# Optimization experiments

Hardware: AMD Instinct MI355X
Metric: run time of the kernel (lower is better)

## Reference

```python
import jax, jax.numpy as jnp
import numpy as np
from math import sqrt

B, N, DK = 4, 4096, 64


def setup_inputs() -> dict:
    key = jax.random.key(0)
    ks = jax.random.split(key, 5)
    x = jax.random.normal(ks[0], (B, N, DK), dtype=jnp.float32)
    Wv = jax.random.normal(ks[1], (DK, DK), dtype=jnp.float32) / sqrt(DK)
    bv = jax.random.normal(ks[2], (DK,), dtype=jnp.float32) * 0.02
    wq = jax.random.normal(ks[3], (DK,), dtype=jnp.float32) / sqrt(DK)
    wk = jax.random.normal(ks[4], (DK,), dtype=jnp.float32) / sqrt(DK)
    gamma = jnp.ones((DK,), dtype=jnp.float32)
    beta = jnp.zeros((DK,), dtype=jnp.float32)
    return {"x": x, "Wv": Wv, "bv": bv, "wq": wq, "wk": wk, "gamma": gamma, "beta": beta}


def _layer_norm(h, gamma, beta, eps=1e-5):
    mu = jnp.mean(h, axis=-1, keepdims=True)
    var = jnp.var(h, axis=-1, keepdims=True)
    return (h - mu) * jax.lax.rsqrt(var + eps) * gamma + beta


def reference(x, Wv, bv, wq, wk, gamma, beta):
    d_k = x.shape[-1]
    V = jnp.einsum('bnd,ed->bne', x, Wv) + bv          # (B, N, DK)
    Q = jnp.einsum('bnd,d->bn', x, wq)                 # scalar per token
    K = jnp.einsum('bnd,d->bn', x, wk)
    # RBF-kernel scores A[b,i,j] = exp(-(Q_i - K_j)^2)  -> (B, N, N)
    A = jnp.exp(-jnp.square(Q[:, :, None] - K[:, None, :]))
    P = jax.nn.softmax(A / sqrt(d_k), axis=-1)
    out = jnp.einsum('bij,bjd->bid', P, V) + x
    return _layer_norm(out, gamma, beta)
```

## Files before the change

kernel.cpp:

```cpp
#include <hip/hip_runtime.h>

#define NB   4
#define NSEQ 4096
#define DK   64
#define NTOK (NB * NSEQ)

#define QK_SCALE 1.2011224087864498f

typedef __attribute__((ext_vector_type(8))) short short8;
typedef __attribute__((ext_vector_type(4))) float f32x4;

__device__ __forceinline__ float fast_exp2(float x) {
#if __has_builtin(__builtin_amdgcn_exp2f)
    return __builtin_amdgcn_exp2f(x);
#else
    return exp2f(x);
#endif
}

__device__ __forceinline__ unsigned short bf16_rne(float f) {
    unsigned u = __float_as_uint(f);
    u += 0x7fffu + ((u >> 16) & 1u);
    return (unsigned short)(u >> 16);
}

__device__ __forceinline__ short8 u4_to_s8(uint4 u) {
    union { uint4 u; short8 s; } c; c.u = u; return c.s;
}

#define AS3U(p) ((__attribute__((address_space(3))) unsigned int*)(p))
#define AS1U(p) ((const __attribute__((address_space(1))) unsigned int*)(p))


__global__ __launch_bounds__(512) void qkv_kernel(
    const float* __restrict__ x, const float* __restrict__ Wv,
    const float* __restrict__ bv, const float* __restrict__ wq,
    const float* __restrict__ wk,
    float* __restrict__ Qs, float* __restrict__ Ks, unsigned short* __restrict__ Vt)
{
    __shared__ float x_lds[64 * 68];
    __shared__ float wvt[64 * 68];
    __shared__ float wqk[128];
    __shared__ float bvl[64];
    __shared__ unsigned short vt_lds[64 * 72];

    const int t = threadIdx.x;
    const int tok0 = blockIdx.x * 64;

    #pragma unroll
    for (int r = 0; r < 2; ++r) {
        int f = t + 512 * r;
        int row = f >> 4, c4 = f & 15;
        float4 v = ((const float4*)(x + (size_t)(tok0 + row) * DK))[c4];
        *(float4*)&x_lds[row * 68 + c4 * 4] = v;
    }
    #pragma unroll
    for (int r = 0; r < 2; ++r) {
        int f = t + 512 * r;
        int e = f >> 4, c4 = f & 15;
        float4 v = ((const float4*)(Wv + e * DK))[c4];
        wvt[(c4 * 4 + 0) * 68 + e] = v.x;
        wvt[(c4 * 4 + 1) * 68 + e] = v.y;
        wvt[(c4 * 4 + 2) * 68 + e] = v.z;
        wvt[(c4 * 4 + 3) * 68 + e] = v.w;
    }
    if (t < 64) { wqk[t * 2] = wq[t]; wqk[t * 2 + 1] = wk[t]; bvl[t] = bv[t]; }
    __syncthreads();

    const int tok = t >> 3, oc = t & 7;
    const int e0 = oc * 8;
    float acc[8];
    #pragma unroll
    for (int ee = 0; ee < 8; ++ee) acc[ee] = bvl[e0 + ee];

    for (int d = 0; d < DK; d += 4) {
        float4 x4 = *(const float4*)&x_lds[tok * 68 + d];
        const float xs[4] = {x4.x, x4.y, x4.z, x4.w};
        #pragma unroll
        for (int dd = 0; dd < 4; ++dd) {
            float xv = xs[dd];
            const float4* wrow = (const float4*)&wvt[(d + dd) * 68 + e0];
            float4 wa = wrow[0], wb = wrow[1];
            acc[0] += xv * wa.x; acc[1] += xv * wa.y;
            acc[2] += xv * wa.z; acc[3] += xv * wa.w;
            acc[4] += xv * wb.x; acc[5] += xv * wb.y;
            acc[6] += xv * wb.z; acc[7] += xv * wb.w;
        }
    }
    #pragma unroll
    for (int k = 0; k < 8; ++k)
        vt_lds[(e0 + k) * 72 + tok] = bf16_rne(acc[k]);

    if (t < 128) {
        const int tk = t & 63;
        const int sel = (t >= 64);
        float a = 0.f;
        for (int d = 0; d < DK; ++d)
            a += x_lds[tk * 68 + d] * wqk[d * 2 + sel];
        (sel ? Ks : Qs)[tok0 + tk] = a * QK_SCALE;
    }
    __syncthreads();

    const int bb = tok0 >> 12, n0 = tok0 & 4095;
    {
        const int c = t >> 6, d = t & 63;
        uint4 v = *(const uint4*)((const char*)vt_lds + d * 144 + c * 16);
        const int jc   = (n0 >> 5) + (c >> 2);
        const int lane = (c & 3) * 16 + (d & 15);
        const int ct   = d >> 4;
        unsigned short* dst = Vt + ((((size_t)bb * 128 + jc) * 4 + ct) * 64 + lane) * 8;
        *(uint4*)dst = v;
    }
}

extern __shared__ float smem[];

__global__ __launch_bounds__(1024, 4) void attn_kernel(
    const float* __restrict__ x,
    const float* __restrict__ Qsg, const float* __restrict__ Ksg,
    const unsigned short* __restrict__ Vt,
    const float* __restrict__ gamma, const float* __restrict__ beta,
    float* __restrict__ out, int nrep)
{
    float* k_lds = smem;
    unsigned short* vs = (unsigned short*)(smem + 4096);
    float* red   = smem + 4096;
    float* dred  = smem + 4096 + 8 * 64 * 68;

    const int t    = threadIdx.x;
    const int B    = blockIdx.x;
    const int b    = (B & 7) >> 1;
    const int i0   = (((B >> 3) << 1) | (B & 1)) << 6;
    const int w    = t >> 6;
    const int lane = t & 63;
    const int rit  = lane & 15;
    const int q    = lane >> 4;
    const int rgrp = w >> 3;
    const int js   = w & 7;

    ((float4*)k_lds)[t] = ((const float4*)(Ksg + (size_t)b * 4096))[t];

    const float Qs0 = Qsg[b * 4096 + i0 + rgrp * 32 + rit];
    const float Qs1 = Qsg[b * 4096 + i0 + rgrp * 32 + 16 + rit];

    const short onebf = (short)0x3F80;
    const short8 vones = {onebf, onebf, onebf, onebf, onebf, onebf, onebf, onebf};

    const unsigned short* Vtb0 = Vt + (size_t)b * 262144;

    for (int rep = 0; rep < nrep; ++rep) {

    f32x4 acc[2][4] = {};
    f32x4 accd[2] = {};

    #pragma unroll
    for (int i = 0; i < 4; ++i) {
        const int row = w + 16 * i;
        const unsigned short* g = Vtb0 + row * 512 + lane * 8;
        unsigned short* l = vs + row * 512;
#if __has_builtin(__builtin_amdgcn_global_load_lds)
        __builtin_amdgcn_global_load_lds(AS1U(g), AS3U(l), 16, 0, 0);
#else
        *(uint4*)(l + lane * 8) = *(const uint4*)g;
#endif
    }
    __syncthreads();

    for (int r = 0; r < 8; ++r) {
        const int bf = r & 1;
        if (r < 7) {
            #pragma unroll
            for (int i = 0; i < 4; ++i) {
                const int row = w + 16 * i;
                const unsigned short* g = Vtb0 + (r + 1) * 32768 + row * 512 + lane * 8;
                unsigned short* l = vs + (bf ^ 1) * 32768 + row * 512;
#if __has_builtin(__builtin_amdgcn_global_load_lds)
                __builtin_amdgcn_global_load_lds(AS1U(g), AS3U(l), 16, 0, 0);
#else
                *(uint4*)(l + lane * 8) = *(const uint4*)g;
#endif
            }
        }

        #pragma unroll
        for (int sl = 0; sl < 2; ++sl) {
            const int jcl = js * 2 + sl;
            const unsigned short* vf = vs + bf * 32768 + jcl * 2048 + lane * 8;
            uint4 bu0 = *(const uint4*)(vf);
            uint4 bu1 = *(const uint4*)(vf + 512);
            uint4 bu2 = *(const uint4*)(vf + 1024);
            uint4 bu3 = *(const uint4*)(vf + 1536);

            const float* kn = k_lds + r * 512 + jcl * 32 + q * 8;
            float4 ka = *(const float4*)(kn);
            float4 kb = *(const float4*)(kn + 4);
            float kv[8] = {ka.x, ka.y, ka.z, ka.w, kb.x, kb.y, kb.z, kb.w};

            float w0[8], w1[8];
            #pragma unroll
            for (int jj = 0; jj < 8; ++jj) {
                float d0 = Qs0 - kv[jj];
                float g0 = fast_exp2(-d0 * d0);
                float p0 = __builtin_fmaf(g0, 3.2552083e-4f, 7.8125e-3f);
                p0 = __builtin_fmaf(g0, p0, 0.125f);
                w0[jj] = __builtin_fmaf(g0, p0, 1.0f);
                float d1 = Qs1 - kv[jj];
                float g1 = fast_exp2(-d1 * d1);
                float p1 = __builtin_fmaf(g1, 3.2552083e-4f, 7.8125e-3f);
                p1 = __builtin_fmaf(g1, p1, 0.125f);
                w1[jj] = __builtin_fmaf(g1, p1, 1.0f);
            }
            uint4 au0, au1;
            au0.x = __builtin_amdgcn_perm(__float_as_uint(w0[1]), __float_as_uint(w0[0]), 0x07060302u);
            au0.y = __builtin_amdgcn_perm(__float_as_uint(w0[3]), __float_as_uint(w0[2]), 0x07060302u);
            au0.z = __builtin_amdgcn_perm(__float_as_uint(w0[5]), __float_as_uint(w0[4]), 0x07060302u);
            au0.w = __builtin_amdgcn_perm(__float_as_uint(w0[7]), __float_as_uint(w0[6]), 0x07060302u);
            au1.x = __builtin_amdgcn_perm(__float_as_uint(w1[1]), __float_as_uint(w1[0]), 0x07060302u);
            au1.y = __builtin_amdgcn_perm(__float_as_uint(w1[3]), __float_as_uint(w1[2]), 0x07060302u);
            au1.z = __builtin_amdgcn_perm(__float_as_uint(w1[5]), __float_as_uint(w1[4]), 0x07060302u);
            au1.w = __builtin_amdgcn_perm(__float_as_uint(w1[7]), __float_as_uint(w1[6]), 0x07060302u);
            short8 a0 = u4_to_s8(au0);
            short8 a1 = u4_to_s8(au1);

            short8 b0 = u4_to_s8(bu0), b1 = u4_to_s8(bu1);
            short8 b2 = u4_to_s8(bu2), b3 = u4_to_s8(bu3);
            acc[0][0] = __builtin_amdgcn_mfma_f32_16x16x32_bf16(a0, b0, acc[0][0], 0, 0, 0);
            acc[0][1] = __builtin_amdgcn_mfma_f32_16x16x32_bf16(a0, b1, acc[0][1], 0, 0, 0);
            acc[0][2] = __builtin_amdgcn_mfma_f32_16x16x32_bf16(a0, b2, acc[0][2], 0, 0, 0);
            acc[0][3] = __builtin_amdgcn_mfma_f32_16x16x32_bf16(a0, b3, acc[0][3], 0, 0, 0);
            acc[1][0] = __builtin_amdgcn_mfma_f32_16x16x32_bf16(a1, b0, acc[1][0], 0, 0, 0);
            acc[1][1] = __builtin_amdgcn_mfma_f32_16x16x32_bf16(a1, b1, acc[1][1], 0, 0, 0);
            acc[1][2] = __builtin_amdgcn_mfma_f32_16x16x32_bf16(a1, b2, acc[1][2], 0, 0, 0);
            acc[1][3] = __builtin_amdgcn_mfma_f32_16x16x32_bf16(a1, b3, acc[1][3], 0, 0, 0);
            accd[0]   = __builtin_amdgcn_mfma_f32_16x16x32_bf16(a0, vones, accd[0], 0, 0, 0);
            accd[1]   = __builtin_amdgcn_mfma_f32_16x16x32_bf16(a1, vones, accd[1], 0, 0, 0);
        }
        __syncthreads();
    }

    {
        float* rbase = red + (size_t)js * (64 * 68);
        #pragma unroll
        for (int rt = 0; rt < 2; ++rt)
            #pragma unroll
            for (int ct = 0; ct < 4; ++ct)
                #pragma unroll
                for (int rg = 0; rg < 4; ++rg)
                    rbase[(rgrp * 32 + rt * 16 + q * 4 + rg) * 68 + ct * 16 + rit]
                        = acc[rt][ct][rg];
        if (rit == 0) {
            #pragma unroll
            for (int rt = 0; rt < 2; ++rt)
                #pragma unroll
                for (int rg = 0; rg < 4; ++rg)
                    dred[js * 64 + rgrp * 32 + rt * 16 + q * 4 + rg] = accd[rt][rg];
        }
    }
    __syncthreads();

    {
        const int row = t >> 4, cg = t & 15, c0 = cg * 4;
        float dsum = 0.f;
        #pragma unroll
        for (int sl = 0; sl < 8; ++sl) dsum += dred[sl * 64 + row];
        const float inv = 1.0f / dsum;
        const size_t rowg = (size_t)(b * 4096 + i0 + row);

        float4 num = make_float4(0.f, 0.f, 0.f, 0.f);
        #pragma unroll
        for (int sl = 0; sl < 8; ++sl) {
            float4 r4 = *(const float4*)&red[(size_t)sl * (64 * 68) + row * 68 + c0];
            num.x += r4.x; num.y += r4.y; num.z += r4.z; num.w += r4.w;
        }
        const float4 x4 = *(const float4*)(x + rowg * 64 + c0);
        float4 h;
        h.x = num.x * inv + x4.x;
        h.y = num.y * inv + x4.y;
        h.z = num.z * inv + x4.z;
        h.w = num.w * inv + x4.w;

        float sm = h.x + h.y + h.z + h.w;
        float ss = h.x * h.x + h.y * h.y + h.z * h.z + h.w * h.w;
        #pragma unroll
        for (int m = 1; m < 16; m <<= 1) { sm += __shfl_xor(sm, m); ss += __shfl_xor(ss, m); }
        const float mu   = sm * 0.015625f;
        const float var  = ss * 0.015625f - mu * mu;
        const float rstd = rsqrtf(var + 1e-5f);

        const float4 g4 = *(const float4*)(gamma + c0);
        const float4 b4 = *(const float4*)(beta + c0);
        float4 o;
        o.x = (h.x - mu) * rstd * g4.x + b4.x;
        o.y = (h.y - mu) * rstd * g4.y + b4.y;
        o.z = (h.z - mu) * rstd * g4.z + b4.z;
        o.w = (h.w - mu) * rstd * g4.w + b4.w;
        *(float4*)(out + rowg * 64 + c0) = o;
    }
    __syncthreads();
    }
}

extern "C" void kernel_launch(void* const* d_in, const int* in_sizes, int n_in,
                              void* d_out, int out_size, void* d_ws, size_t ws_size,
                              hipStream_t stream)
{
    const float* x     = (const float*)d_in[0];
    const float* Wv    = (const float*)d_in[1];
    const float* bv    = (const float*)d_in[2];
    const float* wq    = (const float*)d_in[3];
    const float* wk    = (const float*)d_in[4];
    const float* gamma = (const float*)d_in[5];
    const float* beta  = (const float*)d_in[6];
    float* out = (float*)d_out;

    float* Qs = (float*)d_ws;
    float* Ks = Qs + NTOK;
    unsigned short* Vt = (unsigned short*)(Ks + NTOK);

    const int attn_lds = 4096 * 4 + 8 * 64 * 68 * 4 + 8 * 64 * 4;
    hipFuncSetAttribute((const void*)attn_kernel,
                        hipFuncAttributeMaxDynamicSharedMemorySize, attn_lds);

    qkv_kernel<<<dim3(NTOK / 64), dim3(512), 0, stream>>>(x, Wv, bv, wq, wk, Qs, Ks, Vt);
    attn_kernel<<<dim3(NB * (NSEQ / 64)), dim3(1024), attn_lds, stream>>>(
        x, Qs, Ks, Vt, gamma, beta, out, 1);
}
```

Measured before the change: 94.85 us.

## Give each wave all 64 rows over one key chunk to reuse V fragments

Each of the 16 waves now owns one 32-key chunk per round and computes all four 16-row tiles, instead of two waves splitting rows over two key chunks each. Each V fragment load from LDS now feeds four row tiles, which cuts LDS reads per MFMA. The cost is more accumulator registers (acc[4][4]) and a two-phase cross-wave reduction. The reduction buffer now overlaps the K/V staging area, with 16 denominator slots, and occupancy is pinned with amdgpu_waves_per_eu.

```diff
diff --git a/kernel.cpp b/kernel.cpp
--- a/kernel.cpp
+++ b/kernel.cpp
@@ -115,7 +115,9 @@
 
 extern __shared__ float smem[];
 
-__global__ __launch_bounds__(1024, 4) void attn_kernel(
+__global__ __launch_bounds__(1024)
+__attribute__((amdgpu_waves_per_eu(4, 4)))
+void attn_kernel(
     const float* __restrict__ x,
     const float* __restrict__ Qsg, const float* __restrict__ Ksg,
     const unsigned short* __restrict__ Vt,
@@ -124,24 +126,24 @@
 {
     float* k_lds = smem;
     unsigned short* vs = (unsigned short*)(smem + 4096);
-    float* red   = smem + 4096;
-    float* dred  = smem + 4096 + 8 * 64 * 68;
+    float* red   = smem;
+    float* dred  = smem + 4096 + 32768;
 
     const int t    = threadIdx.x;
     const int B    = blockIdx.x;
     const int b    = (B & 7) >> 1;
     const int i0   = (((B >> 3) << 1) | (B & 1)) << 6;
-    const int w    = t >> 6;
+    const int js   = t >> 6;
     const int lane = t & 63;
     const int rit  = lane & 15;
     const int q    = lane >> 4;
-    const int rgrp = w >> 3;
-    const int js   = w & 7;
 
     ((float4*)k_lds)[t] = ((const float4*)(Ksg + (size_t)b * 4096))[t];
 
-    const float Qs0 = Qsg[b * 4096 + i0 + rgrp * 32 + rit];
-    const float Qs1 = Qsg[b * 4096 + i0 + rgrp * 32 + 16 + rit];
+    float Qr[4];
+    #pragma unroll
+    for (int rt = 0; rt < 4; ++rt)
+        Qr[rt] = Qsg[b * 4096 + i0 + rt * 16 + rit];
 
     const short onebf = (short)0x3F80;
     const short8 vones = {onebf, onebf, onebf, onebf, onebf, onebf, onebf, onebf};
@@ -150,12 +152,12 @@
 
     for (int rep = 0; rep < nrep; ++rep) {
 
-    f32x4 acc[2][4] = {};
-    f32x4 accd[2] = {};
+    f32x4 acc[4][4] = {};
+    f32x4 accd[4] = {};
 
     #pragma unroll
     for (int i = 0; i < 4; ++i) {
-        const int row = w + 16 * i;
+        const int row = js + 16 * i;
         const unsigned short* g = Vtb0 + row * 512 + lane * 8;
         unsigned short* l = vs + row * 512;
 #if __has_builtin(__builtin_amdgcn_global_load_lds)
@@ -171,7 +173,7 @@
         if (r < 7) {
             #pragma unroll
             for (int i = 0; i < 4; ++i) {
-                const int row = w + 16 * i;
+                const int row = js + 16 * i;
                 const unsigned short* g = Vtb0 + (r + 1) * 32768 + row * 512 + lane * 8;
                 unsigned short* l = vs + (bf ^ 1) * 32768 + row * 512;
 #if __has_builtin(__builtin_amdgcn_global_load_lds)
@@ -182,79 +184,78 @@
             }
         }
 
-        #pragma unroll
-        for (int sl = 0; sl < 2; ++sl) {
-            const int jcl = js * 2 + sl;
-            const unsigned short* vf = vs + bf * 32768 + jcl * 2048 + lane * 8;
+        {
+            const unsigned short* vf = vs + bf * 32768 + js * 2048 + lane * 8;
             uint4 bu0 = *(const uint4*)(vf);
             uint4 bu1 = *(const uint4*)(vf + 512);
             uint4 bu2 = *(const uint4*)(vf + 1024);
             uint4 bu3 = *(const uint4*)(vf + 1536);
 
-            const float* kn = k_lds + r * 512 + jcl * 32 + q * 8;
+            const float* kn = k_lds + r * 512 + js * 32 + q * 8;
             float4 ka = *(const float4*)(kn);
             float4 kb = *(const float4*)(kn + 4);
             float kv[8] = {ka.x, ka.y, ka.z, ka.w, kb.x, kb.y, kb.z, kb.w};
 
-            float w0[8], w1[8];
-            #pragma unroll
-            for (int jj = 0; jj < 8; ++jj) {
-                float d0 = Qs0 - kv[jj];
-                float g0 = fast_exp2(-d0 * d0);
-                float p0 = __builtin_fmaf(g0, 3.2552083e-4f, 7.8125e-3f);
-                p0 = __builtin_fmaf(g0, p0, 0.125f);
-                w0[jj] = __builtin_fmaf(g0, p0, 1.0f);
-                float d1 = Qs1 - kv[jj];
-                float g1 = fast_exp2(-d1 * d1);
-                float p1 = __builtin_fmaf(g1, 3.2552083e-4f, 7.8125e-3f);
-                p1 = __builtin_fmaf(g1, p1, 0.125f);
-                w1[jj] = __builtin_fmaf(g1, p1, 1.0f);
-            }
-            uint4 au0, au1;
-            au0.x = __builtin_amdgcn_perm(__float_as_uint(w0[1]), __float_as_uint(w0[0]), 0x07060302u);
-            au0.y = __builtin_amdgcn_perm(__float_as_uint(w0[3]), __float_as_uint(w0[2]), 0x07060302u);
-            au0.z = __builtin_amdgcn_perm(__float_as_uint(w0[5]), __float_as_uint(w0[4]), 0x07060302u);
-            au0.w = __builtin_amdgcn_perm(__float_as_uint(w0[7]), __float_as_uint(w0[6]), 0x07060302u);
-            au1.x = __builtin_amdgcn_perm(__float_as_uint(w1[1]), __float_as_uint(w1[0]), 0x07060302u);
-            au1.y = __builtin_amdgcn_perm(__float_as_uint(w1[3]), __float_as_uint(w1[2]), 0x07060302u);
-            au1.z = __builtin_amdgcn_perm(__float_as_uint(w1[5]), __float_as_uint(w1[4]), 0x07060302u);
-            au1.w = __builtin_amdgcn_perm(__float_as_uint(w1[7]), __float_as_uint(w1[6]), 0x07060302u);
-            short8 a0 = u4_to_s8(au0);
-            short8 a1 = u4_to_s8(au1);
-
             short8 b0 = u4_to_s8(bu0), b1 = u4_to_s8(bu1);
             short8 b2 = u4_to_s8(bu2), b3 = u4_to_s8(bu3);
-            acc[0][0] = __builtin_amdgcn_mfma_f32_16x16x32_bf16(a0, b0, acc[0][0], 0, 0, 0);
-            acc[0][1] = __builtin_amdgcn_mfma_f32_16x16x32_bf16(a0, b1, acc[0][1], 0, 0, 0);
-            acc[0][2] = __builtin_amdgcn_mfma_f32_16x16x32_bf16(a0, b2, acc[0][2], 0, 0, 0);
-            acc[0][3] = __builtin_amdgcn_mfma_f32_16x16x32_bf16(a0, b3, acc[0][3], 0, 0, 0);
-            acc[1][0] = __builtin_amdgcn_mfma_f32_16x16x32_bf16(a1, b0, acc[1][0], 0, 0, 0);
-            acc[1][1] = __builtin_amdgcn_mfma_f32_16x16x32_bf16(a1, b1, acc[1][1], 0, 0, 0);
-            acc[1][2] = __builtin_amdgcn_mfma_f32_16x16x32_bf16(a1, b2, acc[1][2], 0, 0, 0);
-            acc[1][3] = __builtin_amdgcn_mfma_f32_16x16x32_bf16(a1, b3, acc[1][3], 0, 0, 0);
-            accd[0]   = __builtin_amdgcn_mfma_f32_16x16x32_bf16(a0, vones, accd[0], 0, 0, 0);
-            accd[1]   = __builtin_amdgcn_mfma_f32_16x16x32_bf16(a1, vones, accd[1], 0, 0, 0);
+
+            #pragma unroll
+            for (int rt = 0; rt < 4; ++rt) {
+                float w0[8];
+                #pragma unroll
+                for (int jj = 0; jj < 8; ++jj) {
+                    float d0 = Qr[rt] - kv[jj];
+                    float g0 = fast_exp2(-d0 * d0);
+                    float p0 = __builtin_fmaf(g0, 3.2552083e-4f, 7.8125e-3f);
+                    p0 = __builtin_fmaf(g0, p0, 0.125f);
+                    w0[jj] = __builtin_fmaf(g0, p0, 1.0f);
+                }
+                uint4 au;
+                au.x = __builtin_amdgcn_perm(__float_as_uint(w0[1]), __float_as_uint(w0[0]), 0x07060302u);
+                au.y = __builtin_amdgcn_perm(__float_as_uint(w0[3]), __float_as_uint(w0[2]), 0x07060302u);
+                au.z = __builtin_amdgcn_perm(__float_as_uint(w0[5]), __float_as_uint(w0[4]), 0x07060302u);
+                au.w = __builtin_amdgcn_perm(__float_as_uint(w0[7]), __float_as_uint(w0[6]), 0x07060302u);
+                short8 a0 = u4_to_s8(au);
+
+                acc[rt][0] = __builtin_amdgcn_mfma_f32_16x16x32_bf16(a0, b0, acc[rt][0], 0, 0, 0);
+                acc[rt][1] = __builtin_amdgcn_mfma_f32_16x16x32_bf16(a0, b1, acc[rt][1], 0, 0, 0);
+                acc[rt][2] = __builtin_amdgcn_mfma_f32_16x16x32_bf16(a0, b2, acc[rt][2], 0, 0, 0);
+                acc[rt][3] = __builtin_amdgcn_mfma_f32_16x16x32_bf16(a0, b3, acc[rt][3], 0, 0, 0);
+                accd[rt]   = __builtin_amdgcn_mfma_f32_16x16x32_bf16(a0, vones, accd[rt], 0, 0, 0);
+            }
         }
         __syncthreads();
     }
 
-    {
-        float* rbase = red + (size_t)js * (64 * 68);
-        #pragma unroll
-        for (int rt = 0; rt < 2; ++rt)
+    const int slot = js & 7;
+    float* rbase = red + (size_t)slot * (64 * 68);
+    if (js < 8) {
+        #pragma unroll
+        for (int rt = 0; rt < 4; ++rt)
             #pragma unroll
             for (int ct = 0; ct < 4; ++ct)
                 #pragma unroll
                 for (int rg = 0; rg < 4; ++rg)
-                    rbase[(rgrp * 32 + rt * 16 + q * 4 + rg) * 68 + ct * 16 + rit]
-                        = acc[rt][ct][rg];
-        if (rit == 0) {
-            #pragma unroll
-            for (int rt = 0; rt < 2; ++rt)
+                    rbase[(rt * 16 + q * 4 + rg) * 68 + ct * 16 + rit] = acc[rt][ct][rg];
+    }
+    if (rit == 0) {
+        #pragma unroll
+        for (int rt = 0; rt < 4; ++rt)
+            #pragma unroll
+            for (int rg = 0; rg < 4; ++rg)
+                dred[js * 64 + rt * 16 + q * 4 + rg] = accd[rt][rg];
+    }
+    __syncthreads();
+    if (js >= 8) {
+        #pragma unroll
+        for (int rt = 0; rt < 4; ++rt)
+            #pragma unroll
+            for (int ct = 0; ct < 4; ++ct)
                 #pragma unroll
-                for (int rg = 0; rg < 4; ++rg)
-                    dred[js * 64 + rgrp * 32 + rt * 16 + q * 4 + rg] = accd[rt][rg];
-        }
+                for (int rg = 0; rg < 4; ++rg) {
+                    int idx = (rt * 16 + q * 4 + rg) * 68 + ct * 16 + rit;
+                    rbase[idx] += acc[rt][ct][rg];
+                }
     }
     __syncthreads();
 
@@ -262,7 +263,7 @@
         const int row = t >> 4, cg = t & 15, c0 = cg * 4;
         float dsum = 0.f;
         #pragma unroll
-        for (int sl = 0; sl < 8; ++sl) dsum += dred[sl * 64 + row];
+        for (int sl = 0; sl < 16; ++sl) dsum += dred[sl * 64 + row];
         const float inv = 1.0f / dsum;
         const size_t rowg = (size_t)(b * 4096 + i0 + row);
 
@@ -317,7 +318,7 @@
     float* Ks = Qs + NTOK;
     unsigned short* Vt = (unsigned short*)(Ks + NTOK);
 
-    const int attn_lds = 4096 * 4 + 8 * 64 * 68 * 4 + 8 * 64 * 4;
+    const int attn_lds = (4096 + 32768 + 1024) * 4;
     hipFuncSetAttribute((const void*)attn_kernel,
                         hipFuncAttributeMaxDynamicSharedMemorySize, attn_lds);
 
```

Measured after the change: 106.2 us. 12.0% more time.
